# Performance work log

Hardware: AMD Instinct MI355X
Metric: run time of the kernel (lower is better)

Reference implementation:

```python
import jax, jax.numpy as jnp
from jax import lax
import numpy as np

L = 6            # layer_number
CHEB2 = 4        # chebyshev_number ** 2
C = 4 * CHEB2    # per-block channel size = 16
G = 2 ** L       # final block grid = 64 (freq_len / leftover)


def _pool_avg2(y):
    # AvgPool2d kernel=2 stride=2 (dims always divisible here)
    B, Ch, H, W = y.shape
    return y.reshape(B, Ch, H // 2, 2, W // 2, 2).mean(axis=(3, 5))


def _wrap_pad1(y):
    # period_padding by 1 on bottom/right (circular)
    return jnp.pad(y, ((0, 0), (0, 0), (0, 1), (0, 1)), mode='wrap')


def _conv(x, w, groups=1):
    return lax.conv_general_dilated(x, w, (1, 1), 'VALID', feature_group_count=groups)


def _forward(x, W0, b0, Wr, br, Wft, bft):
    B = x.shape[0]
    z0 = jnp.zeros_like(x)
    # split: real input -> (Re+, Re-, Im+=0, Im-=0) per channel (in_channel=1)
    y = jnp.concatenate([jax.nn.relu(x), jax.nn.relu(-x), z0, z0], axis=1)  # [B,4,64,64]
    # layer 0: kernel (w_h,w_w)=(2,2), 4 -> 4*4*cheb^2 = 64
    y = _conv(y, W0) + b0[None, :, None, None]  # [B,64,63,63]
    y = jax.nn.relu(y)
    y = _pool_avg2(_wrap_pad1(y))               # [B,64,32,32] = 2^(L-1) grid
    # recursion layers: per-block 2x2 conv C -> 4C, batched as grouped conv
    for lyr in range(1, L):
        g = 2 ** lyr
        nb = g * g
        z = _conv(y, Wr[lyr - 1], groups=nb) + br[lyr - 1][None, :, None, None]
        s = z.shape[-1]                          # 2^(L-lyr) - 1
        # grouped-conv channel order [A_y, A_x, y_loc, x_loc, C] ->
        # target block index 2^(lyr+1)*(2*A_y+y_loc) + (2*A_x+x_loc):
        z = z.reshape(B, g, g, 2, 2, C, s, s).transpose(0, 1, 3, 2, 4, 5, 6, 7)
        z = z.reshape(B, nb * 4 * C, s, s)
        z = jax.nn.relu(z)
        y = _pool_avg2(_wrap_pad1(z))            # spatial halves -> 2^(L-lyr-1)
    # FT layer: 4^L blocks, 1x1 conv C -> 4*leftover^2 = 4, spatial is 1x1
    v = y.reshape(B, G * G, C)
    f = jnp.einsum('bnc,noc->bno', v, Wft) + bft[None]  # [B,4096,4]
    f = f.reshape(B, G, G, 4)                            # (ky, kx) frequency grid
    real = f[..., 0] - f[..., 1]
    imag = f[..., 2] - f[..., 3]
    return jnp.stack([real, imag], axis=1)               # [B,2,64,64]


def setup_inputs() -> dict:
    key = jax.random.key(0)
    ks = jax.random.split(key, 16)
    sc = 0.1
    inp = {
        'x':  jax.random.normal(ks[0], (256, 1, 64, 64), jnp.float32),
        'W0': sc * jax.random.normal(ks[1], (64, 4, 2, 2), jnp.float32),
        'b0': sc * jax.random.normal(ks[2], (64,), jnp.float32),
        'Wft': sc * jax.random.normal(ks[3], (4096, 4, 16), jnp.float32),
        'bft': sc * jax.random.normal(ks[4], (4096, 4), jnp.float32),
    }
    for lyr in range(1, L):
        nb = 4 ** lyr
        inp[f'W{lyr}'] = sc * jax.random.normal(ks[4 + 2 * lyr - 1], (nb * 4 * C, C, 2, 2), jnp.float32)
        inp[f'b{lyr}'] = sc * jax.random.normal(ks[4 + 2 * lyr], (nb * 4 * C,), jnp.float32)
    return inp


def reference(x, W0, b0, W1, b1, W2, b2, W3, b3, W4, b4, W5, b5, Wft, bft):
    Wr = (W1, W2, W3, W4, W5)
    br = (b1, b2, b3, b4, b5)
    return _forward(x, W0, b0, Wr, br, Wft, bft)
```

## Files before the change

### kernel.cpp

```cpp
#include <hip/hip_runtime.h>
#include <hip/hip_bf16.h>


typedef __attribute__((ext_vector_type(4))) float f32x4;
typedef __attribute__((ext_vector_type(8))) short s16x8;

__device__ __forceinline__ short f2bf(float f) {
  union { float f; unsigned u; } v; v.f = f;
  unsigned r = v.u + 0x7fff + ((v.u >> 16) & 1);
  return (short)(r >> 16);
}
__device__ __forceinline__ float bf2f(short s) {
  union { unsigned u; float f; } v; v.u = ((unsigned)(unsigned short)s) << 16;
  return v.f;
}

__global__ __launch_bounds__(256) void k_layer0(
    const float* __restrict__ x, const float* __restrict__ W0,
    const float* __restrict__ b0, short* __restrict__ out) {
  __shared__ __align__(16) float xs[17 * 64];
  const int b = blockIdx.x, p0 = blockIdx.y * 8;
  const float* xb = x + (size_t)b * 4096;
  for (int i = threadIdx.x; i < 17 * 16; i += 256) {
    int lr = i >> 4, c4 = i & 15;
    ((float4*)xs)[i] = *(const float4*)(xb + ((2 * p0 + lr) & 63) * 64 + c4 * 4);
  }
  __syncthreads();
  const int oc = threadIdx.x & 63, wv = threadIdx.x >> 6;
  float wp[2][2], wm[2][2];
#pragma unroll
  for (int kh = 0; kh < 2; ++kh)
#pragma unroll
    for (int kw = 0; kw < 2; ++kw) {
      wp[kh][kw] = W0[((oc * 4 + 0) * 2 + kh) * 2 + kw];
      wm[kh][kw] = W0[((oc * 4 + 1) * 2 + kh) * 2 + kw];
    }
  const float bias = b0[oc];
  short* ob = out + ((size_t)b * 4 + (oc >> 4)) * 16384 + (oc & 15);
  for (int t = wv; t < 64; t += 4) {
    const int phl = t >> 3, c0 = (t & 7) * 8;
    const int lrA = 2 * phl;
    float vA[9], vB[9], vC[9];
#pragma unroll
    for (int j = 0; j < 8; ++j) {
      vA[j] = xs[lrA * 64 + c0 + j];
      vB[j] = xs[(lrA + 1) * 64 + c0 + j];
      vC[j] = xs[(lrA + 2) * 64 + c0 + j];
    }
    vA[8] = xs[lrA * 64 + ((c0 + 8) & 63)];
    vB[8] = xs[(lrA + 1) * 64 + ((c0 + 8) & 63)];
    vC[8] = xs[(lrA + 2) * 64 + ((c0 + 8) & 63)];
    float pA[9], mA[9], pB[9], mB[9], pC[9], mC[9];
#pragma unroll
    for (int j = 0; j < 9; ++j) {
      pA[j] = fmaxf(vA[j], 0.f); mA[j] = pA[j] - vA[j];
      pB[j] = fmaxf(vB[j], 0.f); mB[j] = pB[j] - vB[j];
      pC[j] = fmaxf(vC[j], 0.f); mC[j] = pC[j] - vC[j];
    }
    float sc0[8], sc1[8];
#pragma unroll
    for (int q = 0; q < 8; ++q) {
      sc0[q] = bias + wp[0][0] * pA[q] + wm[0][0] * mA[q] + wp[0][1] * pA[q + 1] + wm[0][1] * mA[q + 1]
                    + wp[1][0] * pB[q] + wm[1][0] * mB[q] + wp[1][1] * pB[q + 1] + wm[1][1] * mB[q + 1];
      sc1[q] = bias + wp[0][0] * pB[q] + wm[0][0] * mB[q] + wp[0][1] * pB[q + 1] + wm[0][1] * mB[q + 1]
                    + wp[1][0] * pC[q] + wm[1][0] * mC[q] + wp[1][1] * pC[q + 1] + wm[1][1] * mC[q + 1];
    }
#pragma unroll
    for (int p = 0; p < 4; ++p) {
      float po = 0.25f * (fmaxf(sc0[2 * p], 0.f) + fmaxf(sc0[2 * p + 1], 0.f) +
                          fmaxf(sc1[2 * p], 0.f) + fmaxf(sc1[2 * p + 1], 0.f));
      ob[((p0 + phl) * 32 + c0 / 2 + p) * 16] = f2bf(po);
    }
  }
}

template <int S, int G, int IMB>
__global__ __launch_bounds__(256) void k_bconv(
    const short* __restrict__ yin, const float* __restrict__ W,
    const float* __restrict__ Bv, short* __restrict__ yout) {
  constexpr int NB = G * G;
  constexpr int SO = S / 2;
  constexpr int LOG_SO = (SO == 16) ? 4 : (SO == 8) ? 3 : (SO == 4) ? 2 : (SO == 2) ? 1 : 0;
  constexpr int SP = S + 1;
  constexpr int IMG_PIX = SP * SP;
  constexpr int ITERS = IMB * SO * SO / 64;
  __shared__ __align__(16) short ins[IMB * IMG_PIX * 16];
  __shared__ __align__(16) short wl[4096];
  const int gi = blockIdx.x;
  const int b0 = blockIdx.y * IMB;
  const int tid = threadIdx.x;

  const float* wsrc = W + (size_t)gi * 4096;
  for (int i = tid; i < 4096; i += 256) {
    int j = i & 7, row = (i >> 3) & 15, g = (i >> 7) & 3, dy = (i >> 9) & 1, t = i >> 10;
    int k = 8 * g + j;
    int ic = k & 15, dx = k >> 4;
    wl[i] = f2bf(wsrc[((t * 16 + row) * 16 + ic) * 4 + dy * 2 + dx]);
  }
  constexpr int GRAN = IMB * IMG_PIX * 2;
  for (int i = tid; i < GRAN; i += 256) {
    int half = i & 1, q = i >> 1;
    int xx = q % SP; int t2 = q / SP; int yy = t2 % SP; int bi = t2 / SP;
    size_t src = (((size_t)(b0 + bi) * NB + gi) * (S * S) + (yy & (S - 1)) * S + (xx & (S - 1))) * 16 + half * 8;
    *(float4*)&ins[(size_t)q * 16 + half * 8] = *(const float4*)&yin[src];
  }
  __syncthreads();

  const int lane = tid & 63, wv = tid >> 6;
  const int lp = lane & 15, g4 = lane >> 4;
  const int dxg = g4 >> 1, ich = g4 & 1;

  s16x8 af[4][2];
#pragma unroll
  for (int t = 0; t < 4; ++t)
#pragma unroll
    for (int dy = 0; dy < 2; ++dy)
      af[t][dy] = *(const s16x8*)&wl[(((t * 2 + dy) * 4 + g4) * 16 + lp) * 8];
  f32x4 bv[4];
#pragma unroll
  for (int t = 0; t < 4; ++t)
    bv[t] = *(const f32x4*)&Bv[(size_t)gi * 64 + t * 16 + g4 * 4];

  const int A_y = gi / G, A_x = gi - A_y * G;

  for (int it = 0; it < ITERS; ++it) {
    const int pg = it * 64 + wv * 16 + lp;
    const int px = pg & (SO - 1);
    const int py = (pg >> LOG_SO) & (SO - 1);
    const int bi = pg >> (2 * LOG_SO);
    const short* pb = ins + ((size_t)bi * IMG_PIX + (2 * py) * SP + 2 * px + dxg) * 16 + ich * 8;
    const short* r0 = pb;
    const short* r1 = pb + SP * 16;
    const short* r2 = pb + 2 * SP * 16;
    f32x4 acc[4][4];
#pragma unroll
    for (int t = 0; t < 4; ++t)
#pragma unroll
      for (int ph = 0; ph < 4; ++ph) acc[t][ph] = bv[t];
#pragma unroll
    for (int phy = 0; phy < 2; ++phy)
#pragma unroll
      for (int phx = 0; phx < 2; ++phx) {
        const int ph = phy * 2 + phx;
#pragma unroll
        for (int dy = 0; dy < 2; ++dy) {
          const short* rp = (phy + dy == 0) ? r0 : (phy + dy == 1) ? r1 : r2;
          s16x8 bf = *(const s16x8*)(rp + phx * 16);
#pragma unroll
          for (int t = 0; t < 4; ++t)
            acc[t][ph] = __builtin_amdgcn_mfma_f32_16x16x32_bf16(af[t][dy], bf, acc[t][ph], 0, 0, 0);
        }
      }
    const int b = b0 + bi;
#pragma unroll
    for (int t = 0; t < 4; ++t) {
      short pk[4];
#pragma unroll
      for (int r = 0; r < 4; ++r) {
        float po = 0.25f * (fmaxf(acc[t][0][r], 0.f) + fmaxf(acc[t][1][r], 0.f) +
                            fmaxf(acc[t][2][r], 0.f) + fmaxf(acc[t][3][r], 0.f));
        pk[r] = f2bf(po);
      }
      const int gip = (A_y * 2 + (t >> 1)) * (2 * G) + A_x * 2 + (t & 1);
      size_t dst = (((size_t)b * (4 * NB) + gip) * (SO * SO) + py * SO + px) * 16 + g4 * 4;
      *(short4*)&yout[dst] = make_short4(pk[0], pk[1], pk[2], pk[3]);
    }
  }
}

__global__ __launch_bounds__(256) void k_ft(
    const short* __restrict__ v, const float* __restrict__ Wft,
    const float* __restrict__ bft, float* __restrict__ out) {
  const int idx = blockIdx.x * 256 + threadIdx.x;
  const int b = idx >> 12;
  const int n = idx & 4095;
  const short* vp = v + ((size_t)b * 4096 + n) * 16;
  s16x8 a0 = *(const s16x8*)vp;
  s16x8 a1 = *(const s16x8*)(vp + 8);
  float vv[16];
#pragma unroll
  for (int j = 0; j < 8; ++j) { vv[j] = bf2f(a0[j]); vv[8 + j] = bf2f(a1[j]); }
  const float* wp = Wft + (size_t)n * 64;
  float f[4];
#pragma unroll
  for (int o = 0; o < 4; o++) {
    float s = bft[n * 4 + o];
#pragma unroll
    for (int j = 0; j < 16; ++j) s += vv[j] * wp[o * 16 + j];
    f[o] = s;
  }
  out[(size_t)b * 8192 + n] = f[0] - f[1];
  out[(size_t)b * 8192 + 4096 + n] = f[2] - f[3];
}

extern "C" void kernel_launch(void* const* d_in, const int* in_sizes, int n_in,
                              void* d_out, int out_size, void* d_ws, size_t ws_size,
                              hipStream_t stream) {
  const float* x   = (const float*)d_in[0];
  const float* W0  = (const float*)d_in[1];
  const float* b0  = (const float*)d_in[2];
  const float* Wft = (const float*)d_in[3];
  const float* bft = (const float*)d_in[4];
  const float* W1 = (const float*)d_in[5];  const float* b1 = (const float*)d_in[6];
  const float* W2 = (const float*)d_in[7];  const float* b2 = (const float*)d_in[8];
  const float* W3 = (const float*)d_in[9];  const float* b3 = (const float*)d_in[10];
  const float* W4 = (const float*)d_in[11]; const float* b4 = (const float*)d_in[12];
  const float* W5 = (const float*)d_in[13]; const float* b5 = (const float*)d_in[14];

  short* buf0 = (short*)d_ws;
  short* buf1 = buf0 + (size_t)16777216;

  k_layer0<<<dim3(256, 4), 256, 0, stream>>>(x, W0, b0, buf0);
  k_bconv<32, 2, 1><<<dim3(4, 256), 256, 0, stream>>>(buf0, W1, b1, buf1);
  k_bconv<16, 4, 4><<<dim3(16, 64), 256, 0, stream>>>(buf1, W2, b2, buf0);
  k_bconv<8, 8, 16><<<dim3(64, 16), 256, 0, stream>>>(buf0, W3, b3, buf1);
  k_bconv<4, 16, 32><<<dim3(256, 8), 256, 0, stream>>>(buf1, W4, b4, buf0);
  k_bconv<2, 32, 128><<<dim3(1024, 2), 256, 0, stream>>>(buf0, W5, b5, buf1);
  k_ft<<<4096, 256, 0, stream>>>(buf1, Wft, bft, (float*)d_out);
}
```

Measured before the change: 286.8 us.

## Stage layer0 output in LDS, split bconv rows, reuse FT weights across batches

Layer0 now writes its pooled bf16 output into shared memory and then stores it to global with coalesced 16-byte writes, replacing scattered 2-byte stores. The block conv kernel gains a row-tile parameter so each block loads only a band of rows, with a reordered grid (batch fastest) and a fully unrolled pixel loop. This yields more, smaller blocks for the early layers. The FT kernel keeps each frequency's 64 weights in registers and loops over 8 batch items, cutting repeated weight loads at the cost of higher register pressure.

```diff
diff --git a/kernel.cpp b/kernel.cpp
--- a/kernel.cpp
+++ b/kernel.cpp
@@ -14,11 +14,14 @@
   union { unsigned u; float f; } v; v.u = ((unsigned)(unsigned short)s) << 16;
   return v.f;
 }
+constexpr int ilog2c(int v) { return v <= 1 ? 0 : 1 + ilog2c(v / 2); }
 
 __global__ __launch_bounds__(256) void k_layer0(
     const float* __restrict__ x, const float* __restrict__ W0,
     const float* __restrict__ b0, short* __restrict__ out) {
+  constexpr int GS = 4112;
   __shared__ __align__(16) float xs[17 * 64];
+  __shared__ __align__(16) short os[4 * GS];
   const int b = blockIdx.x, p0 = blockIdx.y * 8;
   const float* xb = x + (size_t)b * 4096;
   for (int i = threadIdx.x; i < 17 * 16; i += 256) {
@@ -27,6 +30,7 @@
   }
   __syncthreads();
   const int oc = threadIdx.x & 63, wv = threadIdx.x >> 6;
+  const int g = oc >> 4, c = oc & 15;
   float wp[2][2], wm[2][2];
 #pragma unroll
   for (int kh = 0; kh < 2; ++kh)
@@ -36,7 +40,6 @@
       wm[kh][kw] = W0[((oc * 4 + 1) * 2 + kh) * 2 + kw];
     }
   const float bias = b0[oc];
-  short* ob = out + ((size_t)b * 4 + (oc >> 4)) * 16384 + (oc & 15);
   for (int t = wv; t < 64; t += 4) {
     const int phl = t >> 3, c0 = (t & 7) * 8;
     const int lrA = 2 * phl;
@@ -69,25 +72,35 @@
     for (int p = 0; p < 4; ++p) {
       float po = 0.25f * (fmaxf(sc0[2 * p], 0.f) + fmaxf(sc0[2 * p + 1], 0.f) +
                           fmaxf(sc1[2 * p], 0.f) + fmaxf(sc1[2 * p + 1], 0.f));
-      ob[((p0 + phl) * 32 + c0 / 2 + p) * 16] = f2bf(po);
-    }
-  }
-}
-
-template <int S, int G, int IMB>
+      os[g * GS + (phl * 32 + c0 / 2 + p) * 16 + c] = f2bf(po);
+    }
+  }
+  __syncthreads();
+#pragma unroll
+  for (int gg = 0; gg < 4; ++gg) {
+    short* dst = out + ((size_t)b * 4 + gg) * 16384 + (size_t)p0 * 512;
+    for (int i = threadIdx.x; i < 512; i += 256)
+      *(float4*)&dst[i * 8] = *(const float4*)&os[gg * GS + i * 8];
+  }
+}
+
+template <int S, int G, int IMB, int PH>
 __global__ __launch_bounds__(256) void k_bconv(
     const short* __restrict__ yin, const float* __restrict__ W,
     const float* __restrict__ Bv, short* __restrict__ yout) {
   constexpr int NB = G * G;
   constexpr int SO = S / 2;
-  constexpr int LOG_SO = (SO == 16) ? 4 : (SO == 8) ? 3 : (SO == 4) ? 2 : (SO == 2) ? 1 : 0;
+  constexpr int LOG_SO = ilog2c(SO);
+  constexpr int LOG_PH = ilog2c(PH);
   constexpr int SP = S + 1;
-  constexpr int IMG_PIX = SP * SP;
-  constexpr int ITERS = IMB * SO * SO / 64;
+  constexpr int ROWS = 2 * PH + 1;
+  constexpr int IMG_PIX = ROWS * SP;
+  constexpr int ITERS = IMB * PH * SO / 64;
   __shared__ __align__(16) short ins[IMB * IMG_PIX * 16];
   __shared__ __align__(16) short wl[4096];
-  const int gi = blockIdx.x;
-  const int b0 = blockIdx.y * IMB;
+  const int gi = blockIdx.y;
+  const int b0 = blockIdx.x * IMB;
+  const int p0 = blockIdx.z * PH;
   const int tid = threadIdx.x;
 
   const float* wsrc = W + (size_t)gi * 4096;
@@ -100,8 +113,10 @@
   constexpr int GRAN = IMB * IMG_PIX * 2;
   for (int i = tid; i < GRAN; i += 256) {
     int half = i & 1, q = i >> 1;
-    int xx = q % SP; int t2 = q / SP; int yy = t2 % SP; int bi = t2 / SP;
-    size_t src = (((size_t)(b0 + bi) * NB + gi) * (S * S) + (yy & (S - 1)) * S + (xx & (S - 1))) * 16 + half * 8;
+    int xx = q % SP; int t2 = q / SP; int lr = t2 % ROWS; int bi2 = t2 / ROWS;
+    int gr = (2 * p0 + lr) & (S - 1);
+    int gx = xx & (S - 1);
+    size_t src = (((size_t)(b0 + bi2) * NB + gi) * (S * S) + gr * S + gx) * 16 + half * 8;
     *(float4*)&ins[(size_t)q * 16 + half * 8] = *(const float4*)&yin[src];
   }
   __syncthreads();
@@ -123,12 +138,14 @@
 
   const int A_y = gi / G, A_x = gi - A_y * G;
 
+#pragma unroll
   for (int it = 0; it < ITERS; ++it) {
     const int pg = it * 64 + wv * 16 + lp;
     const int px = pg & (SO - 1);
-    const int py = (pg >> LOG_SO) & (SO - 1);
-    const int bi = pg >> (2 * LOG_SO);
-    const short* pb = ins + ((size_t)bi * IMG_PIX + (2 * py) * SP + 2 * px + dxg) * 16 + ich * 8;
+    const int pyl = (pg >> LOG_SO) & (PH - 1);
+    const int bi = pg >> (LOG_SO + LOG_PH);
+    const int py = p0 + pyl;
+    const short* pb = ins + ((size_t)(bi * ROWS + 2 * pyl) * SP + 2 * px + dxg) * 16 + ich * 8;
     const short* r0 = pb;
     const short* r1 = pb + SP * 16;
     const short* r2 = pb + 2 * SP * 16;
@@ -171,26 +188,36 @@
 __global__ __launch_bounds__(256) void k_ft(
     const short* __restrict__ v, const float* __restrict__ Wft,
     const float* __restrict__ bft, float* __restrict__ out) {
-  const int idx = blockIdx.x * 256 + threadIdx.x;
-  const int b = idx >> 12;
-  const int n = idx & 4095;
-  const short* vp = v + ((size_t)b * 4096 + n) * 16;
-  s16x8 a0 = *(const s16x8*)vp;
-  s16x8 a1 = *(const s16x8*)(vp + 8);
-  float vv[16];
-#pragma unroll
-  for (int j = 0; j < 8; ++j) { vv[j] = bf2f(a0[j]); vv[8 + j] = bf2f(a1[j]); }
-  const float* wp = Wft + (size_t)n * 64;
-  float f[4];
-#pragma unroll
-  for (int o = 0; o < 4; o++) {
-    float s = bft[n * 4 + o];
-#pragma unroll
-    for (int j = 0; j < 16; ++j) s += vv[j] * wp[o * 16 + j];
-    f[o] = s;
-  }
-  out[(size_t)b * 8192 + n] = f[0] - f[1];
-  out[(size_t)b * 8192 + 4096 + n] = f[2] - f[3];
+  const int n = blockIdx.x * 64 + (threadIdx.x & 63);
+  const int b0 = blockIdx.y * 32 + (threadIdx.x >> 6) * 8;
+  float w[64];
+  const float4* wp = (const float4*)(Wft + (size_t)n * 64);
+#pragma unroll
+  for (int j = 0; j < 16; ++j) {
+    float4 t = wp[j];
+    w[4 * j] = t.x; w[4 * j + 1] = t.y; w[4 * j + 2] = t.z; w[4 * j + 3] = t.w;
+  }
+  const float4 bq = *(const float4*)(bft + (size_t)n * 4);
+#pragma unroll 2
+  for (int bb = 0; bb < 8; ++bb) {
+    const int b = b0 + bb;
+    const short* vp = v + ((size_t)b * 4096 + n) * 16;
+    s16x8 a0 = *(const s16x8*)vp;
+    s16x8 a1 = *(const s16x8*)(vp + 8);
+    float vv[16];
+#pragma unroll
+    for (int j = 0; j < 8; ++j) { vv[j] = bf2f(a0[j]); vv[8 + j] = bf2f(a1[j]); }
+    float f0 = bq.x, f1 = bq.y, f2 = bq.z, f3 = bq.w;
+#pragma unroll
+    for (int j = 0; j < 16; ++j) {
+      f0 += vv[j] * w[j];
+      f1 += vv[j] * w[16 + j];
+      f2 += vv[j] * w[32 + j];
+      f3 += vv[j] * w[48 + j];
+    }
+    out[(size_t)b * 8192 + n] = f0 - f1;
+    out[(size_t)b * 8192 + 4096 + n] = f2 - f3;
+  }
 }
 
 extern "C" void kernel_launch(void* const* d_in, const int* in_sizes, int n_in,
@@ -211,10 +238,10 @@
   short* buf1 = buf0 + (size_t)16777216;
 
   k_layer0<<<dim3(256, 4), 256, 0, stream>>>(x, W0, b0, buf0);
-  k_bconv<32, 2, 1><<<dim3(4, 256), 256, 0, stream>>>(buf0, W1, b1, buf1);
-  k_bconv<16, 4, 4><<<dim3(16, 64), 256, 0, stream>>>(buf1, W2, b2, buf0);
-  k_bconv<8, 8, 16><<<dim3(64, 16), 256, 0, stream>>>(buf0, W3, b3, buf1);
-  k_bconv<4, 16, 32><<<dim3(256, 8), 256, 0, stream>>>(buf1, W4, b4, buf0);
-  k_bconv<2, 32, 128><<<dim3(1024, 2), 256, 0, stream>>>(buf0, W5, b5, buf1);
-  k_ft<<<4096, 256, 0, stream>>>(buf1, Wft, bft, (float*)d_out);
-}
+  k_bconv<32, 2, 1, 4><<<dim3(256, 4, 4), 256, 0, stream>>>(buf0, W1, b1, buf1);
+  k_bconv<16, 4, 4, 4><<<dim3(64, 16, 2), 256, 0, stream>>>(buf1, W2, b2, buf0);
+  k_bconv<8, 8, 8, 4><<<dim3(32, 64, 1), 256, 0, stream>>>(buf0, W3, b3, buf1);
+  k_bconv<4, 16, 32, 2><<<dim3(8, 256, 1), 256, 0, stream>>>(buf1, W4, b4, buf0);
+  k_bconv<2, 32, 128, 1><<<dim3(2, 1024, 1), 256, 0, stream>>>(buf0, W5, b5, buf1);
+  k_ft<<<dim3(64, 8), 256, 0, stream>>>(buf1, Wft, bft, (float*)d_out);
+}
```

Result: faster. 269.5 us (-6.0%).
